# Optimization experiments

Measured on AMD Instinct MI355X. Metric: run time of the kernel, lower is better.

Reference implementation:

```python
import jax, jax.numpy as jnp
import numpy as np

B, T, D, H = 4, 2048, 512, 8
HD = D // H  # head_dim = 64


def setup_inputs() -> dict:
    key = jax.random.key(0)
    k1, k2, k3 = jax.random.split(key, 3)
    x = jax.random.normal(k1, (B, T, D), dtype=jnp.float32)
    # causal lower-triangular mask; positions with 0 are masked to -inf
    attn_mask = jnp.tril(jnp.ones((T, T), dtype=jnp.int32))
    Wqkv = jax.random.normal(k2, (D, 3 * D), dtype=jnp.float32) * (1.0 / np.sqrt(D))
    Wout = jax.random.normal(k3, (D, D), dtype=jnp.float32) * (1.0 / np.sqrt(D))
    return {"x": x, "attn_mask": attn_mask, "Wqkv": Wqkv, "Wout": Wout}


def reference(x, attn_mask, Wqkv, Wout):
    # qkv projection (bias=False)
    qkv = x @ Wqkv                               # [B,T,3D]
    q, k, v = jnp.split(qkv, 3, axis=-1)          # each [B,T,D]

    def heads(t):
        return t.reshape(B, T, H, HD).transpose(0, 2, 1, 3)  # [B,H,T,HD]

    q, k, v = heads(q), heads(k), heads(v)
    scale = 1.0 / np.sqrt(HD)
    att = jnp.einsum('bhqd,bhkd->bhqk', q, k) * scale         # [B,H,T,T]
    att = jnp.where(attn_mask[None, None, :, :] == 0, -jnp.inf, att)
    att = jax.nn.softmax(att, axis=-1)
    # dropout p=0.0 (eval): identity
    y = jnp.einsum('bhqk,bhkd->bhqd', att, v)                 # [B,H,T,HD]
    y = y.transpose(0, 2, 1, 3).reshape(B, T, D)
    return y @ Wout
```

## Files before the change

kernel.cpp:

```cpp
#include <hip/hip_runtime.h>

#define NB 4
#define NT 2048
#define ND 512
#define NH 8
#define NHD 64

typedef __attribute__((ext_vector_type(4))) float f32x4;
typedef __attribute__((ext_vector_type(8))) short bf16x8;
typedef __attribute__((ext_vector_type(4))) short bf16x4;
typedef __attribute__((ext_vector_type(4))) unsigned int u32x4;
typedef __attribute__((ext_vector_type(2))) unsigned int u32x2;

__device__ __forceinline__ unsigned short f2bf(float f) {
    unsigned u = __builtin_bit_cast(unsigned, f);
    u += 0x7FFFu + ((u >> 16) & 1u);
    return (unsigned short)(u >> 16);
}
__device__ __forceinline__ float bf2f(unsigned short h) {
    unsigned u = ((unsigned)h) << 16;
    return __builtin_bit_cast(float, u);
}
__device__ __forceinline__ float exp2_fast(float x) {
    float r;
    asm("v_exp_f32 %0, %1" : "=v"(r) : "v"(x));
    return r;
}
__device__ __forceinline__ unsigned cvt_pk_bf16(float lo, float hi) {
    unsigned r;
    asm("v_cvt_pk_bf16_f32 %0, %1, %2" : "=v"(r) : "v"(lo), "v"(hi));
    return r;
}

#define GLOAD16(g, s)                                                          \
    __builtin_amdgcn_global_load_lds(                                          \
        (const __attribute__((address_space(1))) unsigned int*)(g),            \
        (__attribute__((address_space(3))) unsigned int*)(s), 16, 0, 0)

__global__ __launch_bounds__(256) void k_cvt(const float* __restrict__ in,
                                             unsigned short* __restrict__ out, int n8) {
    int i = blockIdx.x * 256 + threadIdx.x;
    if (i >= n8) return;
    const float* p = in + (long)i * 8;
    f32x4 a = *(const f32x4*)p;
    f32x4 b = *(const f32x4*)(p + 4);
    bf16x8 o;
#pragma unroll
    for (int e = 0; e < 4; e++) {
        o[e] = (short)f2bf(a[e]);
        o[e + 4] = (short)f2bf(b[e]);
    }
    *(bf16x8*)(out + (long)i * 8) = o;
}

__global__ __launch_bounds__(256) void k_tr(const float* __restrict__ in,
                                            unsigned short* __restrict__ out, int R, int C) {
    __shared__ unsigned short tile[32][33];
    int c0 = blockIdx.x * 32, r0 = blockIdx.y * 32;
    int tx = threadIdx.x, ty = threadIdx.y;
#pragma unroll
    for (int j = 0; j < 32; j += 8)
        tile[ty + j][tx] = f2bf(in[(long)(r0 + ty + j) * C + c0 + tx]);
    __syncthreads();
#pragma unroll
    for (int j = 0; j < 32; j += 8)
        out[(long)(c0 + ty + j) * R + r0 + tx] = tile[tx][ty + j];
}

template <int EPI>
__global__ __launch_bounds__(256) void k_gemm(const unsigned short* __restrict__ A,
                                              const unsigned short* __restrict__ Bt,
                                              float* __restrict__ outf,
                                              unsigned short* __restrict__ q,
                                              unsigned short* __restrict__ kk_,
                                              unsigned short* __restrict__ vt,
                                              int M, int N, int K) {
    __shared__ unsigned short Al[128 * 64];
    __shared__ unsigned short Bl[128 * 64];
    int id = blockIdx.x;
    int xcd = id & 7, s = id >> 3;
    int ytile = (s & 7) * 8 + xcd;
    int xtile = s >> 3;
    int m0 = ytile * 128, n0 = xtile * 128;
    int tid = threadIdx.x;
    int w = tid >> 6, l = tid & 63;
    int wm = (w >> 1) * 64, wn = (w & 1) * 64;
    int lr = l & 15, lg = l >> 4;

    f32x4 acc[4][4];
#pragma unroll
    for (int i = 0; i < 4; i++)
#pragma unroll
        for (int j = 0; j < 4; j++) acc[i][j] = (f32x4){0.f, 0.f, 0.f, 0.f};

    for (int k0 = 0; k0 < K; k0 += 64) {
        __syncthreads();
#pragma unroll
        for (int p = 0; p < 4; p++) {
            int c = p * 256 + tid;
            int row = c >> 3, ch = c & 7;
            u32x4 va = *(const u32x4*)(A + (long)(m0 + row) * K + k0 + ch * 8);
            *(u32x4*)(Al + row * 64 + ((ch ^ (row & 7)) * 8)) = va;
            u32x4 vb = *(const u32x4*)(Bt + (long)(n0 + row) * K + k0 + ch * 8);
            *(u32x4*)(Bl + row * 64 + ((ch ^ (row & 7)) * 8)) = vb;
        }
        __syncthreads();
#pragma unroll
        for (int kc = 0; kc < 2; kc++) {
            bf16x8 af[4], bff[4];
#pragma unroll
            for (int i = 0; i < 4; i++) {
                int row = wm + i * 16 + lr;
                int ch = (kc * 4 + lg) ^ (row & 7);
                af[i] = *(const bf16x8*)(Al + row * 64 + ch * 8);
                int rowb = wn + i * 16 + lr;
                int chb = (kc * 4 + lg) ^ (rowb & 7);
                bff[i] = *(const bf16x8*)(Bl + rowb * 64 + chb * 8);
            }
#pragma unroll
            for (int i = 0; i < 4; i++)
#pragma unroll
                for (int j = 0; j < 4; j++)
                    acc[i][j] = __builtin_amdgcn_mfma_f32_16x16x32_bf16(af[i], bff[j], acc[i][j], 0, 0, 0);
        }
    }

    if (EPI == 0) {
#pragma unroll
        for (int i = 0; i < 4; i++)
#pragma unroll
            for (int j = 0; j < 4; j++) {
                int row = m0 + wm + i * 16 + lg * 4;
                int col = n0 + wn + j * 16 + lr;
#pragma unroll
                for (int r = 0; r < 4; r++) outf[(long)(row + r) * N + col] = acc[i][j][r];
            }
    } else {
#pragma unroll
        for (int i = 0; i < 4; i++)
#pragma unroll
            for (int j = 0; j < 4; j++) {
                int m = m0 + wm + i * 16 + lg * 4;
                int col = n0 + wn + j * 16 + lr;
                int sel = col >> 9;
                int cc = col & 511;
                int h = cc >> 6, hd = cc & 63;
                int b = m >> 11, t = m & 2047;
                long bh = (long)(b * NH + h);
                if (sel == 0) {
#pragma unroll
                    for (int r = 0; r < 4; r++)
                        q[(bh * NT + t + r) * NHD + hd] = f2bf(acc[i][j][r]);
                } else if (sel == 1) {
#pragma unroll
                    for (int r = 0; r < 4; r++)
                        kk_[(bh * NT + t + r) * NHD + hd] = f2bf(acc[i][j][r]);
                } else {
                    bf16x4 pk;
#pragma unroll
                    for (int r = 0; r < 4; r++) pk[r] = (short)f2bf(acc[i][j][r]);
                    *(bf16x4*)(vt + (bh * NHD + hd) * NT + t) = pk;
                }
            }
    }
}

__global__ __launch_bounds__(256, 4) void k_attn(const unsigned short* __restrict__ qb,
                                                 const unsigned short* __restrict__ kb,
                                                 const unsigned short* __restrict__ vtb,
                                                 unsigned short* __restrict__ yb) {
    __shared__ unsigned short Kl[2][64 * 64];
    __shared__ unsigned short Vl[2][64 * 64];
    __shared__ unsigned short Pl[4 * 16 * 64];

    int id = blockIdx.x;
    int xcd = id & 7, s = id >> 3;
    int bh = (s & 3) * 8 + xcd;
    int qt = 31 - (s >> 2);
    int q0 = qt * 64;
    int nkt = qt + 1;

    int tid = threadIdx.x, w = tid >> 6, l = tid & 63;
    int lr = l & 15, lg = l >> 4;
    int lrow8 = l >> 3, lch = l & 7;
    int chg = lch ^ lrow8;
    long hbase = (long)bh * NT * NHD;
    const float QSCALE = 0.125f * 1.4426950408889634f;

    int qrow = q0 + w * 16 + lr;
    bf16x8 qf[2];
#pragma unroll
    for (int dh = 0; dh < 2; dh++) {
        bf16x8 v = *(const bf16x8*)(qb + hbase + (long)qrow * NHD + dh * 32 + lg * 8);
#pragma unroll
        for (int e = 0; e < 8; e++) v[e] = (short)f2bf(bf2f((unsigned short)v[e]) * QSCALE);
        qf[dh] = v;
    }

    float mrun = -__builtin_inff(), ell = 0.f;
    f32x4 ot[4];
#pragma unroll
    for (int i = 0; i < 4; i++) ot[i] = (f32x4){0.f, 0.f, 0.f, 0.f};

    {
#pragma unroll
        for (int j = 0; j < 2; j++) {
            int br = w * 16 + j * 8;
            GLOAD16(kb + hbase + (long)(br + lrow8) * NHD + chg * 8, &Kl[0][br * 64]);
            GLOAD16(vtb + hbase + (long)(br + lrow8) * NT + chg * 8, &Vl[0][br * 64]);
        }
    }

    for (int kt = 0; kt < nkt; kt++) {
        int b = kt & 1;
        __syncthreads();
        if (kt + 1 < nkt) {
            int k0s = (kt + 1) * 64;
#pragma unroll
            for (int j = 0; j < 2; j++) {
                int br = w * 16 + j * 8;
                GLOAD16(kb + hbase + (long)(k0s + br + lrow8) * NHD + chg * 8,
                        &Kl[b ^ 1][br * 64]);
                GLOAD16(vtb + hbase + (long)(br + lrow8) * NT + k0s + chg * 8,
                        &Vl[b ^ 1][br * 64]);
            }
        }
        int k0 = kt * 64;
        const unsigned short* Kb = Kl[b];
        const unsigned short* Vb = Vl[b];

        f32x4 st[4];
        __builtin_amdgcn_s_setprio(1);
#pragma unroll
        for (int sub = 0; sub < 4; sub++) {
            f32x4 z = (f32x4){0.f, 0.f, 0.f, 0.f};
#pragma unroll
            for (int dh = 0; dh < 2; dh++) {
                int row = sub * 16 + lr;
                int ch = (dh * 4 + lg) ^ (row & 7);
                bf16x8 kf = *(const bf16x8*)(Kb + row * 64 + ch * 8);
                z = __builtin_amdgcn_mfma_f32_16x16x32_bf16(kf, qf[dh], z, 0, 0, 0);
            }
            st[sub] = z;
        }
        __builtin_amdgcn_s_setprio(0);

        if (kt == nkt - 1) {
            int qg = q0 + w * 16 + lr;
#pragma unroll
            for (int sub = 0; sub < 4; sub++)
#pragma unroll
                for (int r = 0; r < 4; r++) {
                    int tg = k0 + sub * 16 + lg * 4 + r;
                    if (tg > qg) st[sub][r] = -__builtin_inff();
                }
        }

        float pmax = st[0][0];
#pragma unroll
        for (int sub = 0; sub < 4; sub++)
#pragma unroll
            for (int r = 0; r < 4; r++) pmax = fmaxf(pmax, st[sub][r]);
        pmax = fmaxf(pmax, __shfl_xor(pmax, 16));
        pmax = fmaxf(pmax, __shfl_xor(pmax, 32));

        if (!__all(pmax - mrun <= 8.f)) {
            float mn = fmaxf(mrun, pmax);
            float alpha = exp2_fast(mrun - mn);
            ell *= alpha;
#pragma unroll
            for (int sub = 0; sub < 4; sub++) ot[sub] *= alpha;
            mrun = mn;
        }

        float psum = 0.f;
#pragma unroll
        for (int sub = 0; sub < 4; sub++) {
            float p0 = exp2_fast(st[sub][0] - mrun);
            float p1 = exp2_fast(st[sub][1] - mrun);
            float p2 = exp2_fast(st[sub][2] - mrun);
            float p3 = exp2_fast(st[sub][3] - mrun);
            psum += (p0 + p1) + (p2 + p3);
            u32x2 pw;
            pw[0] = cvt_pk_bf16(p0, p1);
            pw[1] = cvt_pk_bf16(p2, p3);
            int t = sub * 16 + lg * 4;
            int ch = t >> 3;
            *(u32x2*)(Pl + w * 1024 + lr * 64 + ((ch ^ (lr & 7)) * 8) + (t & 7)) = pw;
        }
        psum += __shfl_xor(psum, 16);
        psum += __shfl_xor(psum, 32);
        ell += psum;

        bf16x8 pf[2];
#pragma unroll
        for (int th = 0; th < 2; th++) {
            int ch = (th * 4 + lg) ^ (lr & 7);
            pf[th] = *(const bf16x8*)(Pl + w * 1024 + lr * 64 + ch * 8);
        }
        __builtin_amdgcn_s_setprio(1);
#pragma unroll
        for (int md = 0; md < 4; md++) {
#pragma unroll
            for (int th = 0; th < 2; th++) {
                int row = md * 16 + lr;
                int ch = (th * 4 + lg) ^ (row & 7);
                bf16x8 vf = *(const bf16x8*)(Vb + row * 64 + ch * 8);
                ot[md] = __builtin_amdgcn_mfma_f32_16x16x32_bf16(vf, pf[th], ot[md], 0, 0, 0);
            }
        }
        __builtin_amdgcn_s_setprio(0);
    }

    float inv = 1.f / ell;
    long yrow = (long)((bh >> 3) * NT + q0 + w * 16 + lr);
    int hcol = (bh & 7) * NHD;
#pragma unroll
    for (int sub = 0; sub < 4; sub++) {
        bf16x4 o;
#pragma unroll
        for (int r = 0; r < 4; r++) o[r] = (short)f2bf(ot[sub][r] * inv);
        *(bf16x4*)(yb + yrow * ND + hcol + sub * 16 + lg * 4) = o;
    }
}

extern "C" void kernel_launch(void* const* d_in, const int* in_sizes, int n_in,
                              void* d_out, int out_size, void* d_ws, size_t ws_size,
                              hipStream_t stream) {
    const float* x = (const float*)d_in[0];
    const float* Wqkv = (const float*)d_in[2];
    const float* Wout = (const float*)d_in[3];

    char* ws = (char*)d_ws;
    unsigned short* xb = (unsigned short*)(ws);
    unsigned short* wqkvt = (unsigned short*)(ws + 8388608);
    unsigned short* woutt = (unsigned short*)(ws + 8388608 + 1572864);
    unsigned short* qb = (unsigned short*)(ws + 10485760);
    unsigned short* kb = (unsigned short*)(ws + 10485760 + 8388608);
    unsigned short* vtb = (unsigned short*)(ws + 10485760 + 16777216);
    unsigned short* yb = xb;
    float* out = (float*)d_out;

    k_cvt<<<dim3(2048), dim3(256), 0, stream>>>(x, xb, (NB * NT * ND) / 8);
    k_tr<<<dim3(48, 16), dim3(32, 8), 0, stream>>>(Wqkv, wqkvt, 512, 1536);
    k_tr<<<dim3(16, 16), dim3(32, 8), 0, stream>>>(Wout, woutt, 512, 512);
    k_gemm<1><<<dim3(768), dim3(256), 0, stream>>>(xb, wqkvt, nullptr, qb, kb, vtb,
                                                   NB * NT, 3 * ND, ND);
    k_attn<<<dim3(1024), dim3(256), 0, stream>>>(qb, kb, vtb, yb);
    k_gemm<0><<<dim3(256), dim3(256), 0, stream>>>(yb, woutt, out, nullptr, nullptr, nullptr,
                                                   NB * NT, ND, ND);
}
```

Baseline: 159.4 us.

## Process two query sub-tiles per wave in attention; use direct global-to-LDS loads in GEMM

The attention kernel now runs 128 threads per block, and each of the two waves handles 32 query rows as two 16-row sub-tiles. Each K and V fragment read from LDS therefore feeds two MFMAs, which halves LDS read traffic per unit of compute and doubles register accumulators. The GEMM tile staging switches from register-staged vector loads with swizzled stores to the GLOAD16 direct-to-LDS path. The trade-off is higher register pressure and fewer waves per block for load issue, with possible occupancy loss.

```diff
diff --git a/kernel.cpp b/kernel.cpp
--- a/kernel.cpp
+++ b/kernel.cpp
@@ -86,6 +86,8 @@
     int w = tid >> 6, l = tid & 63;
     int wm = (w >> 1) * 64, wn = (w & 1) * 64;
     int lr = l & 15, lg = l >> 4;
+    int lrow8 = l >> 3, lch = l & 7;
+    int chg = lch ^ lrow8;
 
     f32x4 acc[4][4];
 #pragma unroll
@@ -97,12 +99,10 @@
         __syncthreads();
 #pragma unroll
         for (int p = 0; p < 4; p++) {
-            int c = p * 256 + tid;
-            int row = c >> 3, ch = c & 7;
-            u32x4 va = *(const u32x4*)(A + (long)(m0 + row) * K + k0 + ch * 8);
-            *(u32x4*)(Al + row * 64 + ((ch ^ (row & 7)) * 8)) = va;
-            u32x4 vb = *(const u32x4*)(Bt + (long)(n0 + row) * K + k0 + ch * 8);
-            *(u32x4*)(Bl + row * 64 + ((ch ^ (row & 7)) * 8)) = vb;
+            int br = p * 32 + w * 8;
+            int row = br + lrow8;
+            GLOAD16(A + (long)(m0 + row) * K + k0 + chg * 8, &Al[br * 64]);
+            GLOAD16(Bt + (long)(n0 + row) * K + k0 + chg * 8, &Bl[br * 64]);
         }
         __syncthreads();
 #pragma unroll
@@ -165,7 +165,7 @@
     }
 }
 
-__global__ __launch_bounds__(256, 4) void k_attn(const unsigned short* __restrict__ qb,
+__global__ __launch_bounds__(128, 2) void k_attn(const unsigned short* __restrict__ qb,
                                                  const unsigned short* __restrict__ kb,
                                                  const unsigned short* __restrict__ vtb,
                                                  unsigned short* __restrict__ yb) {
@@ -187,28 +187,32 @@
     long hbase = (long)bh * NT * NHD;
     const float QSCALE = 0.125f * 1.4426950408889634f;
 
-    int qrow = q0 + w * 16 + lr;
-    bf16x8 qf[2];
-#pragma unroll
-    for (int dh = 0; dh < 2; dh++) {
-        bf16x8 v = *(const bf16x8*)(qb + hbase + (long)qrow * NHD + dh * 32 + lg * 8);
-#pragma unroll
-        for (int e = 0; e < 8; e++) v[e] = (short)f2bf(bf2f((unsigned short)v[e]) * QSCALE);
-        qf[dh] = v;
-    }
-
-    float mrun = -__builtin_inff(), ell = 0.f;
-    f32x4 ot[4];
-#pragma unroll
-    for (int i = 0; i < 4; i++) ot[i] = (f32x4){0.f, 0.f, 0.f, 0.f};
-
-    {
-#pragma unroll
-        for (int j = 0; j < 2; j++) {
-            int br = w * 16 + j * 8;
-            GLOAD16(kb + hbase + (long)(br + lrow8) * NHD + chg * 8, &Kl[0][br * 64]);
-            GLOAD16(vtb + hbase + (long)(br + lrow8) * NT + chg * 8, &Vl[0][br * 64]);
-        }
+    bf16x8 qf[2][2];
+#pragma unroll
+    for (int qbk = 0; qbk < 2; qbk++) {
+        int qrow = q0 + w * 32 + qbk * 16 + lr;
+#pragma unroll
+        for (int dh = 0; dh < 2; dh++) {
+            bf16x8 v = *(const bf16x8*)(qb + hbase + (long)qrow * NHD + dh * 32 + lg * 8);
+#pragma unroll
+            for (int e = 0; e < 8; e++) v[e] = (short)f2bf(bf2f((unsigned short)v[e]) * QSCALE);
+            qf[qbk][dh] = v;
+        }
+    }
+
+    float mrun[2] = {-__builtin_inff(), -__builtin_inff()};
+    float ell[2] = {0.f, 0.f};
+    f32x4 ot[2][4];
+#pragma unroll
+    for (int qbk = 0; qbk < 2; qbk++)
+#pragma unroll
+        for (int i = 0; i < 4; i++) ot[qbk][i] = (f32x4){0.f, 0.f, 0.f, 0.f};
+
+#pragma unroll
+    for (int j = 0; j < 4; j++) {
+        int br = w * 32 + j * 8;
+        GLOAD16(kb + hbase + (long)(br + lrow8) * NHD + chg * 8, &Kl[0][br * 64]);
+        GLOAD16(vtb + hbase + (long)(br + lrow8) * NT + chg * 8, &Vl[0][br * 64]);
     }
 
     for (int kt = 0; kt < nkt; kt++) {
@@ -217,8 +221,8 @@
         if (kt + 1 < nkt) {
             int k0s = (kt + 1) * 64;
 #pragma unroll
-            for (int j = 0; j < 2; j++) {
-                int br = w * 16 + j * 8;
+            for (int j = 0; j < 4; j++) {
+                int br = w * 32 + j * 8;
                 GLOAD16(kb + hbase + (long)(k0s + br + lrow8) * NHD + chg * 8,
                         &Kl[b ^ 1][br * 64]);
                 GLOAD16(vtb + hbase + (long)(br + lrow8) * NT + k0s + chg * 8,
@@ -229,75 +233,96 @@
         const unsigned short* Kb = Kl[b];
         const unsigned short* Vb = Vl[b];
 
-        f32x4 st[4];
+        f32x4 st[2][4];
         __builtin_amdgcn_s_setprio(1);
 #pragma unroll
         for (int sub = 0; sub < 4; sub++) {
-            f32x4 z = (f32x4){0.f, 0.f, 0.f, 0.f};
+            f32x4 z0 = (f32x4){0.f, 0.f, 0.f, 0.f};
+            f32x4 z1 = (f32x4){0.f, 0.f, 0.f, 0.f};
 #pragma unroll
             for (int dh = 0; dh < 2; dh++) {
                 int row = sub * 16 + lr;
                 int ch = (dh * 4 + lg) ^ (row & 7);
                 bf16x8 kf = *(const bf16x8*)(Kb + row * 64 + ch * 8);
-                z = __builtin_amdgcn_mfma_f32_16x16x32_bf16(kf, qf[dh], z, 0, 0, 0);
-            }
-            st[sub] = z;
+                z0 = __builtin_amdgcn_mfma_f32_16x16x32_bf16(kf, qf[0][dh], z0, 0, 0, 0);
+                z1 = __builtin_amdgcn_mfma_f32_16x16x32_bf16(kf, qf[1][dh], z1, 0, 0, 0);
+            }
+            st[0][sub] = z0;
+            st[1][sub] = z1;
         }
         __builtin_amdgcn_s_setprio(0);
 
         if (kt == nkt - 1) {
-            int qg = q0 + w * 16 + lr;
+#pragma unroll
+            for (int qbk = 0; qbk < 2; qbk++) {
+                int qg = q0 + w * 32 + qbk * 16 + lr;
+#pragma unroll
+                for (int sub = 0; sub < 4; sub++)
+#pragma unroll
+                    for (int r = 0; r < 4; r++) {
+                        int tg = k0 + sub * 16 + lg * 4 + r;
+                        if (tg > qg) st[qbk][sub][r] = -__builtin_inff();
+                    }
+            }
+        }
+
+        float pmax[2];
+#pragma unroll
+        for (int qbk = 0; qbk < 2; qbk++) {
+            float pm = st[qbk][0][0];
 #pragma unroll
             for (int sub = 0; sub < 4; sub++)
 #pragma unroll
-                for (int r = 0; r < 4; r++) {
-                    int tg = k0 + sub * 16 + lg * 4 + r;
-                    if (tg > qg) st[sub][r] = -__builtin_inff();
-                }
-        }
-
-        float pmax = st[0][0];
-#pragma unroll
-        for (int sub = 0; sub < 4; sub++)
-#pragma unroll
-            for (int r = 0; r < 4; r++) pmax = fmaxf(pmax, st[sub][r]);
-        pmax = fmaxf(pmax, __shfl_xor(pmax, 16));
-        pmax = fmaxf(pmax, __shfl_xor(pmax, 32));
-
-        if (!__all(pmax - mrun <= 8.f)) {
-            float mn = fmaxf(mrun, pmax);
-            float alpha = exp2_fast(mrun - mn);
-            ell *= alpha;
-#pragma unroll
-            for (int sub = 0; sub < 4; sub++) ot[sub] *= alpha;
-            mrun = mn;
-        }
-
-        float psum = 0.f;
-#pragma unroll
-        for (int sub = 0; sub < 4; sub++) {
-            float p0 = exp2_fast(st[sub][0] - mrun);
-            float p1 = exp2_fast(st[sub][1] - mrun);
-            float p2 = exp2_fast(st[sub][2] - mrun);
-            float p3 = exp2_fast(st[sub][3] - mrun);
-            psum += (p0 + p1) + (p2 + p3);
-            u32x2 pw;
-            pw[0] = cvt_pk_bf16(p0, p1);
-            pw[1] = cvt_pk_bf16(p2, p3);
-            int t = sub * 16 + lg * 4;
-            int ch = t >> 3;
-            *(u32x2*)(Pl + w * 1024 + lr * 64 + ((ch ^ (lr & 7)) * 8) + (t & 7)) = pw;
-        }
-        psum += __shfl_xor(psum, 16);
-        psum += __shfl_xor(psum, 32);
-        ell += psum;
-
-        bf16x8 pf[2];
-#pragma unroll
-        for (int th = 0; th < 2; th++) {
-            int ch = (th * 4 + lg) ^ (lr & 7);
-            pf[th] = *(const bf16x8*)(Pl + w * 1024 + lr * 64 + ch * 8);
-        }
+                for (int r = 0; r < 4; r++) pm = fmaxf(pm, st[qbk][sub][r]);
+            pm = fmaxf(pm, __shfl_xor(pm, 16));
+            pm = fmaxf(pm, __shfl_xor(pm, 32));
+            pmax[qbk] = pm;
+        }
+
+        bool ok = (pmax[0] - mrun[0] <= 8.f) && (pmax[1] - mrun[1] <= 8.f);
+        if (!__all(ok)) {
+#pragma unroll
+            for (int qbk = 0; qbk < 2; qbk++) {
+                float mn = fmaxf(mrun[qbk], pmax[qbk]);
+                float alpha = exp2_fast(mrun[qbk] - mn);
+                ell[qbk] *= alpha;
+#pragma unroll
+                for (int sub = 0; sub < 4; sub++) ot[qbk][sub] *= alpha;
+                mrun[qbk] = mn;
+            }
+        }
+
+#pragma unroll
+        for (int qbk = 0; qbk < 2; qbk++) {
+            float psum = 0.f;
+            unsigned short* Ps = Pl + (w * 2 + qbk) * 1024;
+#pragma unroll
+            for (int sub = 0; sub < 4; sub++) {
+                float p0 = exp2_fast(st[qbk][sub][0] - mrun[qbk]);
+                float p1 = exp2_fast(st[qbk][sub][1] - mrun[qbk]);
+                float p2 = exp2_fast(st[qbk][sub][2] - mrun[qbk]);
+                float p3 = exp2_fast(st[qbk][sub][3] - mrun[qbk]);
+                psum += (p0 + p1) + (p2 + p3);
+                u32x2 pw;
+                pw[0] = cvt_pk_bf16(p0, p1);
+                pw[1] = cvt_pk_bf16(p2, p3);
+                int t = sub * 16 + lg * 4;
+                int ch = t >> 3;
+                *(u32x2*)(Ps + lr * 64 + ((ch ^ (lr & 7)) * 8) + (t & 7)) = pw;
+            }
+            psum += __shfl_xor(psum, 16);
+            psum += __shfl_xor(psum, 32);
+            ell[qbk] += psum;
+        }
+
+        bf16x8 pf[2][2];
+#pragma unroll
+        for (int qbk = 0; qbk < 2; qbk++)
+#pragma unroll
+            for (int th = 0; th < 2; th++) {
+                int ch = (th * 4 + lg) ^ (lr & 7);
+                pf[qbk][th] = *(const bf16x8*)(Pl + (w * 2 + qbk) * 1024 + lr * 64 + ch * 8);
+            }
         __builtin_amdgcn_s_setprio(1);
 #pragma unroll
         for (int md = 0; md < 4; md++) {
@@ -306,21 +331,25 @@
                 int row = md * 16 + lr;
                 int ch = (th * 4 + lg) ^ (row & 7);
                 bf16x8 vf = *(const bf16x8*)(Vb + row * 64 + ch * 8);
-                ot[md] = __builtin_amdgcn_mfma_f32_16x16x32_bf16(vf, pf[th], ot[md], 0, 0, 0);
+                ot[0][md] = __builtin_amdgcn_mfma_f32_16x16x32_bf16(vf, pf[0][th], ot[0][md], 0, 0, 0);
+                ot[1][md] = __builtin_amdgcn_mfma_f32_16x16x32_bf16(vf, pf[1][th], ot[1][md], 0, 0, 0);
             }
         }
         __builtin_amdgcn_s_setprio(0);
     }
 
-    float inv = 1.f / ell;
-    long yrow = (long)((bh >> 3) * NT + q0 + w * 16 + lr);
-    int hcol = (bh & 7) * NHD;
-#pragma unroll
-    for (int sub = 0; sub < 4; sub++) {
-        bf16x4 o;
-#pragma unroll
-        for (int r = 0; r < 4; r++) o[r] = (short)f2bf(ot[sub][r] * inv);
-        *(bf16x4*)(yb + yrow * ND + hcol + sub * 16 + lg * 4) = o;
+#pragma unroll
+    for (int qbk = 0; qbk < 2; qbk++) {
+        float inv = 1.f / ell[qbk];
+        long yrow = (long)((bh >> 3) * NT + q0 + w * 32 + qbk * 16 + lr);
+        int hcol = (bh & 7) * NHD;
+#pragma unroll
+        for (int sub = 0; sub < 4; sub++) {
+            bf16x4 o;
+#pragma unroll
+            for (int r = 0; r < 4; r++) o[r] = (short)f2bf(ot[qbk][sub][r] * inv);
+            *(bf16x4*)(yb + yrow * ND + hcol + sub * 16 + lg * 4) = o;
+        }
     }
 }
 
@@ -335,8 +364,8 @@
     unsigned short* xb = (unsigned short*)(ws);
     unsigned short* wqkvt = (unsigned short*)(ws + 8388608);
     unsigned short* woutt = (unsigned short*)(ws + 8388608 + 1572864);
-    unsigned short* qb = (unsigned short*)(ws + 10485760);
-    unsigned short* kb = (unsigned short*)(ws + 10485760 + 8388608);
+    unsigned short* qbp = (unsigned short*)(ws + 10485760);
+    unsigned short* kbp = (unsigned short*)(ws + 10485760 + 8388608);
     unsigned short* vtb = (unsigned short*)(ws + 10485760 + 16777216);
     unsigned short* yb = xb;
     float* out = (float*)d_out;
@@ -344,9 +373,9 @@
     k_cvt<<<dim3(2048), dim3(256), 0, stream>>>(x, xb, (NB * NT * ND) / 8);
     k_tr<<<dim3(48, 16), dim3(32, 8), 0, stream>>>(Wqkv, wqkvt, 512, 1536);
     k_tr<<<dim3(16, 16), dim3(32, 8), 0, stream>>>(Wout, woutt, 512, 512);
-    k_gemm<1><<<dim3(768), dim3(256), 0, stream>>>(xb, wqkvt, nullptr, qb, kb, vtb,
+    k_gemm<1><<<dim3(768), dim3(256), 0, stream>>>(xb, wqkvt, nullptr, qbp, kbp, vtb,
                                                    NB * NT, 3 * ND, ND);
-    k_attn<<<dim3(1024), dim3(256), 0, stream>>>(qb, kb, vtb, yb);
+    k_attn<<<dim3(1024), dim3(128), 0, stream>>>(qbp, kbp, vtb, yb);
     k_gemm<0><<<dim3(256), dim3(256), 0, stream>>>(yb, woutt, out, nullptr, nullptr, nullptr,
                                                    NB * NT, ND, ND);
 }
```

Measured after the change: 167.0 us. 1.05x slower.

## Merge prep kernels, use direct-to-LDS loads, double-buffer output GEMM

Applied to the files above, without the earlier changes.

Combines the x conversion and both weight transposes into one launch, cutting launch overhead. Switches the QKV GEMM tile loads to global_load_lds, with a pre-swizzled source address instead of register staging. Rewrites the output projection GEMM with 64x128 tiles, which doubles its block count for better CU coverage, and adds double-buffered LDS prefetch. This adds code complexity and relies on the per-wave contiguous LDS write pattern of global_load_lds matching the XOR swizzle.

```diff
diff --git a/kernel.cpp b/kernel.cpp
--- a/kernel.cpp
+++ b/kernel.cpp
@@ -37,27 +37,42 @@
         (const __attribute__((address_space(1))) unsigned int*)(g),            \
         (__attribute__((address_space(3))) unsigned int*)(s), 16, 0, 0)
 
-__global__ __launch_bounds__(256) void k_cvt(const float* __restrict__ in,
-                                             unsigned short* __restrict__ out, int n8) {
-    int i = blockIdx.x * 256 + threadIdx.x;
-    if (i >= n8) return;
-    const float* p = in + (long)i * 8;
-    f32x4 a = *(const f32x4*)p;
-    f32x4 b = *(const f32x4*)(p + 4);
-    bf16x8 o;
-#pragma unroll
-    for (int e = 0; e < 4; e++) {
-        o[e] = (short)f2bf(a[e]);
-        o[e + 4] = (short)f2bf(b[e]);
-    }
-    *(bf16x8*)(out + (long)i * 8) = o;
-}
-
-__global__ __launch_bounds__(256) void k_tr(const float* __restrict__ in,
-                                            unsigned short* __restrict__ out, int R, int C) {
+__global__ __launch_bounds__(256) void k_prep(const float* __restrict__ x,
+                                              const float* __restrict__ Wqkv,
+                                              const float* __restrict__ Wout,
+                                              unsigned short* __restrict__ xb,
+                                              unsigned short* __restrict__ wqkvt,
+                                              unsigned short* __restrict__ woutt) {
     __shared__ unsigned short tile[32][33];
-    int c0 = blockIdx.x * 32, r0 = blockIdx.y * 32;
-    int tx = threadIdx.x, ty = threadIdx.y;
+    int id = blockIdx.x;
+    if (id < 2048) {
+        int i = id * 256 + threadIdx.x;
+        const float* p = x + (long)i * 8;
+        f32x4 a = *(const f32x4*)p;
+        f32x4 b = *(const f32x4*)(p + 4);
+        bf16x8 o;
+#pragma unroll
+        for (int e = 0; e < 4; e++) {
+            o[e] = (short)f2bf(a[e]);
+            o[e + 4] = (short)f2bf(b[e]);
+        }
+        *(bf16x8*)(xb + (long)i * 8) = o;
+        return;
+    }
+    const float* in;
+    unsigned short* out;
+    int R, C, bx, by;
+    if (id < 2816) {
+        int t = id - 2048;
+        in = Wqkv; out = wqkvt; R = 512; C = 1536;
+        bx = t % 48; by = t / 48;
+    } else {
+        int t = id - 2816;
+        in = Wout; out = woutt; R = 512; C = 512;
+        bx = t % 16; by = t / 16;
+    }
+    int c0 = bx * 32, r0 = by * 32;
+    int tx = threadIdx.x & 31, ty = threadIdx.x >> 5;
 #pragma unroll
     for (int j = 0; j < 32; j += 8)
         tile[ty + j][tx] = f2bf(in[(long)(r0 + ty + j) * C + c0 + tx]);
@@ -67,14 +82,12 @@
         out[(long)(c0 + ty + j) * R + r0 + tx] = tile[tx][ty + j];
 }
 
-template <int EPI>
-__global__ __launch_bounds__(256) void k_gemm(const unsigned short* __restrict__ A,
-                                              const unsigned short* __restrict__ Bt,
-                                              float* __restrict__ outf,
-                                              unsigned short* __restrict__ q,
-                                              unsigned short* __restrict__ kk_,
-                                              unsigned short* __restrict__ vt,
-                                              int M, int N, int K) {
+__global__ __launch_bounds__(256) void k_gemm1(const unsigned short* __restrict__ A,
+                                               const unsigned short* __restrict__ Bt,
+                                               unsigned short* __restrict__ q,
+                                               unsigned short* __restrict__ kk_,
+                                               unsigned short* __restrict__ vt,
+                                               int K, int N) {
     __shared__ unsigned short Al[128 * 64];
     __shared__ unsigned short Bl[128 * 64];
     int id = blockIdx.x;
@@ -86,6 +99,8 @@
     int w = tid >> 6, l = tid & 63;
     int wm = (w >> 1) * 64, wn = (w & 1) * 64;
     int lr = l & 15, lg = l >> 4;
+    int lrow8 = l >> 3, lch = l & 7;
+    int chg = lch ^ lrow8;
 
     f32x4 acc[4][4];
 #pragma unroll
@@ -97,12 +112,10 @@
         __syncthreads();
 #pragma unroll
         for (int p = 0; p < 4; p++) {
-            int c = p * 256 + tid;
-            int row = c >> 3, ch = c & 7;
-            u32x4 va = *(const u32x4*)(A + (long)(m0 + row) * K + k0 + ch * 8);
-            *(u32x4*)(Al + row * 64 + ((ch ^ (row & 7)) * 8)) = va;
-            u32x4 vb = *(const u32x4*)(Bt + (long)(n0 + row) * K + k0 + ch * 8);
-            *(u32x4*)(Bl + row * 64 + ((ch ^ (row & 7)) * 8)) = vb;
+            int br = p * 32 + w * 8;
+            int row = br + lrow8;
+            GLOAD16(A + (long)(m0 + row) * K + k0 + chg * 8, &Al[br * 64]);
+            GLOAD16(Bt + (long)(n0 + row) * K + k0 + chg * 8, &Bl[br * 64]);
         }
         __syncthreads();
 #pragma unroll
@@ -125,44 +138,120 @@
         }
     }
 
-    if (EPI == 0) {
-#pragma unroll
-        for (int i = 0; i < 4; i++)
+#pragma unroll
+    for (int i = 0; i < 4; i++)
+#pragma unroll
+        for (int j = 0; j < 4; j++) {
+            int m = m0 + wm + i * 16 + lg * 4;
+            int col = n0 + wn + j * 16 + lr;
+            int sel = col >> 9;
+            int cc = col & 511;
+            int h = cc >> 6, hd = cc & 63;
+            int b = m >> 11, t = m & 2047;
+            long bh = (long)(b * NH + h);
+            if (sel == 0) {
+#pragma unroll
+                for (int r = 0; r < 4; r++)
+                    q[(bh * NT + t + r) * NHD + hd] = f2bf(acc[i][j][r]);
+            } else if (sel == 1) {
+#pragma unroll
+                for (int r = 0; r < 4; r++)
+                    kk_[(bh * NT + t + r) * NHD + hd] = f2bf(acc[i][j][r]);
+            } else {
+                bf16x4 pk;
+#pragma unroll
+                for (int r = 0; r < 4; r++) pk[r] = (short)f2bf(acc[i][j][r]);
+                *(bf16x4*)(vt + (bh * NHD + hd) * NT + t) = pk;
+            }
+        }
+}
+
+__global__ __launch_bounds__(256) void k_gemm2(const unsigned short* __restrict__ A,
+                                               const unsigned short* __restrict__ Bt,
+                                               float* __restrict__ outf,
+                                               int K, int N) {
+    __shared__ unsigned short Al[2][64 * 64];
+    __shared__ unsigned short Bl[2][128 * 64];
+    int id = blockIdx.x;
+    int xcd = id & 7, s = id >> 3;
+    int ytile = (s & 15) * 8 + xcd;
+    int xtile = s >> 4;
+    int m0 = ytile * 64, n0 = xtile * 128;
+    int tid = threadIdx.x;
+    int w = tid >> 6, l = tid & 63;
+    int wm = (w >> 1) * 32, wn = (w & 1) * 64;
+    int lr = l & 15, lg = l >> 4;
+    int lrow8 = l >> 3, lch = l & 7;
+    int chg = lch ^ lrow8;
+
+    f32x4 acc[2][4];
+#pragma unroll
+    for (int i = 0; i < 2; i++)
+#pragma unroll
+        for (int j = 0; j < 4; j++) acc[i][j] = (f32x4){0.f, 0.f, 0.f, 0.f};
+
+#pragma unroll
+    for (int j = 0; j < 2; j++) {
+        int br = w * 16 + j * 8;
+        GLOAD16(A + (long)(m0 + br + lrow8) * K + chg * 8, &Al[0][br * 64]);
+    }
+#pragma unroll
+    for (int j = 0; j < 4; j++) {
+        int br = w * 32 + j * 8;
+        GLOAD16(Bt + (long)(n0 + br + lrow8) * K + chg * 8, &Bl[0][br * 64]);
+    }
+
+    int nk = K / 64;
+    for (int kt = 0; kt < nk; kt++) {
+        int cur = kt & 1;
+        __syncthreads();
+        if (kt + 1 < nk) {
+            int k0 = (kt + 1) * 64;
+#pragma unroll
+            for (int j = 0; j < 2; j++) {
+                int br = w * 16 + j * 8;
+                GLOAD16(A + (long)(m0 + br + lrow8) * K + k0 + chg * 8, &Al[cur ^ 1][br * 64]);
+            }
 #pragma unroll
             for (int j = 0; j < 4; j++) {
-                int row = m0 + wm + i * 16 + lg * 4;
-                int col = n0 + wn + j * 16 + lr;
-#pragma unroll
-                for (int r = 0; r < 4; r++) outf[(long)(row + r) * N + col] = acc[i][j][r];
-            }
-    } else {
-#pragma unroll
-        for (int i = 0; i < 4; i++)
+                int br = w * 32 + j * 8;
+                GLOAD16(Bt + (long)(n0 + br + lrow8) * K + k0 + chg * 8, &Bl[cur ^ 1][br * 64]);
+            }
+        }
+        const unsigned short* Ab = Al[cur];
+        const unsigned short* Bb = Bl[cur];
+#pragma unroll
+        for (int kc = 0; kc < 2; kc++) {
+            bf16x8 af[2], bff[4];
+#pragma unroll
+            for (int i = 0; i < 2; i++) {
+                int row = wm + i * 16 + lr;
+                int ch = (kc * 4 + lg) ^ (row & 7);
+                af[i] = *(const bf16x8*)(Ab + row * 64 + ch * 8);
+            }
 #pragma unroll
             for (int j = 0; j < 4; j++) {
-                int m = m0 + wm + i * 16 + lg * 4;
-                int col = n0 + wn + j * 16 + lr;
-                int sel = col >> 9;
-                int cc = col & 511;
-                int h = cc >> 6, hd = cc & 63;
-                int b = m >> 11, t = m & 2047;
-                long bh = (long)(b * NH + h);
-                if (sel == 0) {
-#pragma unroll
-                    for (int r = 0; r < 4; r++)
-                        q[(bh * NT + t + r) * NHD + hd] = f2bf(acc[i][j][r]);
-                } else if (sel == 1) {
-#pragma unroll
-                    for (int r = 0; r < 4; r++)
-                        kk_[(bh * NT + t + r) * NHD + hd] = f2bf(acc[i][j][r]);
-                } else {
-                    bf16x4 pk;
-#pragma unroll
-                    for (int r = 0; r < 4; r++) pk[r] = (short)f2bf(acc[i][j][r]);
-                    *(bf16x4*)(vt + (bh * NHD + hd) * NT + t) = pk;
-                }
-            }
-    }
+                int rowb = wn + j * 16 + lr;
+                int chb = (kc * 4 + lg) ^ (rowb & 7);
+                bff[j] = *(const bf16x8*)(Bb + rowb * 64 + chb * 8);
+            }
+#pragma unroll
+            for (int i = 0; i < 2; i++)
+#pragma unroll
+                for (int j = 0; j < 4; j++)
+                    acc[i][j] = __builtin_amdgcn_mfma_f32_16x16x32_bf16(af[i], bff[j], acc[i][j], 0, 0, 0);
+        }
+    }
+
+#pragma unroll
+    for (int i = 0; i < 2; i++)
+#pragma unroll
+        for (int j = 0; j < 4; j++) {
+            int row = m0 + wm + i * 16 + lg * 4;
+            int col = n0 + wn + j * 16 + lr;
+#pragma unroll
+            for (int r = 0; r < 4; r++) outf[(long)(row + r) * N + col] = acc[i][j][r];
+        }
 }
 
 __global__ __launch_bounds__(256, 4) void k_attn(const unsigned short* __restrict__ qb,
@@ -335,18 +424,14 @@
     unsigned short* xb = (unsigned short*)(ws);
     unsigned short* wqkvt = (unsigned short*)(ws + 8388608);
     unsigned short* woutt = (unsigned short*)(ws + 8388608 + 1572864);
-    unsigned short* qb = (unsigned short*)(ws + 10485760);
-    unsigned short* kb = (unsigned short*)(ws + 10485760 + 8388608);
+    unsigned short* qbp = (unsigned short*)(ws + 10485760);
+    unsigned short* kbp = (unsigned short*)(ws + 10485760 + 8388608);
     unsigned short* vtb = (unsigned short*)(ws + 10485760 + 16777216);
     unsigned short* yb = xb;
     float* out = (float*)d_out;
 
-    k_cvt<<<dim3(2048), dim3(256), 0, stream>>>(x, xb, (NB * NT * ND) / 8);
-    k_tr<<<dim3(48, 16), dim3(32, 8), 0, stream>>>(Wqkv, wqkvt, 512, 1536);
-    k_tr<<<dim3(16, 16), dim3(32, 8), 0, stream>>>(Wout, woutt, 512, 512);
-    k_gemm<1><<<dim3(768), dim3(256), 0, stream>>>(xb, wqkvt, nullptr, qb, kb, vtb,
-                                                   NB * NT, 3 * ND, ND);
-    k_attn<<<dim3(1024), dim3(256), 0, stream>>>(qb, kb, vtb, yb);
-    k_gemm<0><<<dim3(256), dim3(256), 0, stream>>>(yb, woutt, out, nullptr, nullptr, nullptr,
-                                                   NB * NT, ND, ND);
-}
+    k_prep<<<dim3(3072), dim3(256), 0, stream>>>(x, Wqkv, Wout, xb, wqkvt, woutt);
+    k_gemm1<<<dim3(768), dim3(256), 0, stream>>>(xb, wqkvt, qbp, kbp, vtb, ND, 3 * ND);
+    k_attn<<<dim3(1024), dim3(256), 0, stream>>>(qbp, kbp, vtb, yb);
+    k_gemm2<<<dim3(512), dim3(256), 0, stream>>>(yb, woutt, out, ND, ND);
+}
```

Result: faster. 149.4 us (-6.3%).
